# Performance work log

Measured on AMD Instinct MI355X. Metric: run time of the kernel, lower is better.

The kernel has to match this reference:

```python
import jax, jax.numpy as jnp
import numpy as np

B, N, D, E = 2, 50000, 64, 800000


def setup_inputs() -> dict:
    key = jax.random.key(0)
    k = jax.random.split(key, 6)
    return {
        "prev_embeddings": jax.random.normal(k[0], (B, N, D), dtype=jnp.float32),
        "edges_ij": jax.random.randint(k[1], (E, 2), 0, N, dtype=jnp.int64 if jax.config.jax_enable_x64 else jnp.int32),
        "node_features_embeddings": jax.random.normal(k[2], (B, N, D), dtype=jnp.float32),
        "edge_features_embeddings": jax.random.normal(k[3], (B, N, D), dtype=jnp.float32),
        "edge_status": jax.random.uniform(k[4], (E,), dtype=jnp.float32),
        "W": jax.random.normal(k[5], (D, D), dtype=jnp.float32) / np.sqrt(D).astype(np.float32),
    }


def reference(prev_embeddings, edges_ij, node_features_embeddings, edge_features_embeddings, edge_status, W):
    # prev_embeddings: (B, N, D); edges_ij: (E, 2); edge_status: (E,) in [0,1]; W: (D, D) theta2 weight (no bias)
    u = edges_ij[:, 0]
    v = edges_ij[:, 1]
    g = edge_status.astype(prev_embeddings.dtype).reshape(1, -1, 1)  # broadcast (1,E,1) over batch
    h_u = prev_embeddings[:, u, :] * g  # gather source endpoint, gate
    h_v = prev_embeddings[:, v, :] * g  # gather dest endpoint, gate
    # scatter-add gated messages in both directions: nbr[b, v] += h_u, nbr[b, u] += h_v
    nbr = jnp.zeros_like(prev_embeddings).at[:, v, :].add(h_u).at[:, u, :].add(h_v)
    x2 = jnp.einsum('bnd,ed->bne', nbr, W)  # Linear(D,D,bias=False): nbr @ W.T
    return jax.nn.leaky_relu(node_features_embeddings + x2 + edge_features_embeddings)
```

## Files before the change

kernel.cpp:

```cpp
#include <hip/hip_runtime.h>

constexpr int B = 2;
constexpr int N = 50000;
constexpr int D = 64;
constexpr int E = 800000;
constexpr int CAP = 96;
constexpr int XG = 8;
constexpr int NPG = N / XG;
constexpr int CSTRIDE_PAD = 16;

constexpr int ROWS_PER_WAVE = 25;
constexpr int BGROUPS = 1563;
constexpr int PGROUPS = 125;
constexpr int TOTAL_GROUPS = BGROUPS + PGROUPS;

__device__ __forceinline__ unsigned f2bf(float f) {
    unsigned u = __float_as_uint(f);
    return (u + 0x7FFFu + ((u >> 16) & 1u)) >> 16;
}
__device__ __forceinline__ float bfhi2f(unsigned bits) {
    return __uint_as_float(bits & 0xFFFF0000u);
}
__device__ __forceinline__ float bflo2f(unsigned bits) {
    return __uint_as_float(bits << 16);
}

__device__ __forceinline__ void acc8(float g, const uint4& r, float* a) {
    a[0] += g * bflo2f(r.x); a[1] += g * bfhi2f(r.x);
    a[2] += g * bflo2f(r.y); a[3] += g * bfhi2f(r.y);
    a[4] += g * bflo2f(r.z); a[5] += g * bfhi2f(r.z);
    a[6] += g * bflo2f(r.w); a[7] += g * bfhi2f(r.w);
}

__global__ __launch_bounds__(256) void build_pgemm_fused(
    const int2* __restrict__ edges, const float* __restrict__ status,
    int* __restrict__ counts, unsigned* __restrict__ slots,
    const float* __restrict__ prev, const float* __restrict__ W,
    unsigned* __restrict__ P32, int cstride)
{
    int grp = blockIdx.x >> 3;
    int sub8 = blockIdx.x & 7;
    int t = threadIdx.x;

    int cyc = grp / 13, pos = grp % 13;
    bool is_pgemm = (pos == 12) && (grp < PGROUPS * 13);

    if (!is_pgemm) {
        int b = (grp < PGROUPS * 13) ? (cyc * 12 + pos) : (1500 + (grp - PGROUPS * 13));
        int e0 = b * 512 + t;
        int e1 = e0 + 256;
        bool has1 = (e1 < E);

        int2 uv0 = edges[e0];
        float st0 = status[e0];
        int2 uv1 = has1 ? edges[e1] : uv0;
        float st1 = has1 ? status[e1] : 0.f;
        unsigned gb0 = f2bf(st0) << 16;
        unsigned gb1 = f2bf(st1) << 16;

        bool du0 = (uv0.x / NPG == sub8);
        bool dv0 = (uv0.y / NPG == sub8);
        bool du1 = has1 && (uv1.x / NPG == sub8);
        bool dv1 = has1 && (uv1.y / NPG == sub8);

        int pu0 = CAP, pv0 = CAP, pu1 = CAP, pv1 = CAP;
        if (du0) pu0 = atomicAdd(&counts[(size_t)uv0.x * cstride], 1);
        if (dv0) pv0 = atomicAdd(&counts[(size_t)uv0.y * cstride], 1);
        if (du1) pu1 = atomicAdd(&counts[(size_t)uv1.x * cstride], 1);
        if (dv1) pv1 = atomicAdd(&counts[(size_t)uv1.y * cstride], 1);
        if (du0 && pu0 < CAP) slots[(size_t)uv0.x * CAP + pu0] = gb0 | (unsigned)uv0.y;
        if (dv0 && pv0 < CAP) slots[(size_t)uv0.y * CAP + pv0] = gb0 | (unsigned)uv0.x;
        if (du1 && pu1 < CAP) slots[(size_t)uv1.x * CAP + pu1] = gb1 | (unsigned)uv1.y;
        if (dv1 && pv1 < CAP) slots[(size_t)uv1.y * CAP + pv1] = gb1 | (unsigned)uv1.x;
    } else {
        int pb = cyc * 8 + sub8;
        int wave = t >> 6, lane = t & 63;

        const float4* W4 = (const float4*)W;
        float4 w[16];
#pragma unroll
        for (int q = 0; q < 16; ++q) w[q] = W4[lane * 16 + q];

        int row0 = pb * (4 * ROWS_PER_WAVE) + wave * ROWS_PER_WAVE;
        for (int r = 0; r < ROWS_PER_WAVE; ++r) {
            int row = __builtin_amdgcn_readfirstlane(row0 + r);
            const float* pr = prev + (size_t)row * D;

            float acc = 0.f;
#pragma unroll
            for (int d = 0; d < D; ++d) {
                const float4& wq = w[d >> 2];
                float wd = (d & 3) == 0 ? wq.x : (d & 3) == 1 ? wq.y
                         : (d & 3) == 2 ? wq.z : wq.w;
                acc += pr[d] * wd;
            }

            float partner = __shfl_xor(acc, 1, 64);
            if ((lane & 1) == 0) {
                int bsel = row >= N;
                int n = row - bsel * N;
                P32[(size_t)n * 64 + bsel * 32 + (lane >> 1)]
                    = f2bf(acc) | (f2bf(partner) << 16);
            }
        }
    }
}

__global__ __launch_bounds__(256) void gather_final(
    const uint4* __restrict__ P4,
    const int* __restrict__ counts,
    const unsigned* __restrict__ slots,
    const float* __restrict__ node,
    const float* __restrict__ edgef,
    float* __restrict__ out, int cstride)
{
    __shared__ float xs[4][2][D];

    int t = threadIdx.x;
    int wave = t >> 6, lane = t & 63;
    int n = blockIdx.x * 4 + wave;
    int j = lane & 7;
    int sub = lane >> 3;

    size_t b0 = (size_t)n * D + lane;
    size_t b1 = (size_t)N * D + b0;
    float nd0 = __builtin_nontemporal_load(node + b0);
    float ef0 = __builtin_nontemporal_load(edgef + b0);
    float nd1 = __builtin_nontemporal_load(node + b1);
    float ef1 = __builtin_nontemporal_load(edgef + b1);

    int cnt = min(counts[(size_t)n * cstride], CAP);
    size_t sbase = (size_t)n * CAP;

    float a0[8], a1[8];
#pragma unroll
    for (int i = 0; i < 8; ++i) { a0[i] = 0.f; a1[i] = 0.f; }

    int last = cnt - 1;
    int nch = (cnt + 31) >> 5;
    for (int c = 0; c < nch; ++c) {
        int k0 = sub + c * 32;
        unsigned e0 = __builtin_nontemporal_load(slots + sbase + min(k0,      last));
        unsigned e1 = __builtin_nontemporal_load(slots + sbase + min(k0 + 8,  last));
        unsigned e2 = __builtin_nontemporal_load(slots + sbase + min(k0 + 16, last));
        unsigned e3 = __builtin_nontemporal_load(slots + sbase + min(k0 + 24, last));
        float g0 = (k0      < cnt) ? bfhi2f(e0) : 0.f;
        float g1 = (k0 + 8  < cnt) ? bfhi2f(e1) : 0.f;
        float g2 = (k0 + 16 < cnt) ? bfhi2f(e2) : 0.f;
        float g3 = (k0 + 24 < cnt) ? bfhi2f(e3) : 0.f;
        unsigned m0 = e0 & 0xFFFFu, m1 = e1 & 0xFFFFu;
        unsigned m2 = e2 & 0xFFFFu, m3 = e3 & 0xFFFFu;
        uint4 r00 = P4[(size_t)m0 * 16 + j];
        uint4 r10 = P4[(size_t)m0 * 16 + 8 + j];
        uint4 r01 = P4[(size_t)m1 * 16 + j];
        uint4 r11 = P4[(size_t)m1 * 16 + 8 + j];
        uint4 r02 = P4[(size_t)m2 * 16 + j];
        uint4 r12 = P4[(size_t)m2 * 16 + 8 + j];
        uint4 r03 = P4[(size_t)m3 * 16 + j];
        uint4 r13 = P4[(size_t)m3 * 16 + 8 + j];
        acc8(g0, r00, a0); acc8(g0, r10, a1);
        acc8(g1, r01, a0); acc8(g1, r11, a1);
        acc8(g2, r02, a0); acc8(g2, r12, a1);
        acc8(g3, r03, a0); acc8(g3, r13, a1);
    }

#pragma unroll
    for (int m = 8; m <= 32; m <<= 1) {
#pragma unroll
        for (int i = 0; i < 8; ++i) {
            a0[i] += __shfl_xor(a0[i], m, 64);
            a1[i] += __shfl_xor(a1[i], m, 64);
        }
    }

    if (sub == 0) {
        *(float4*)&xs[wave][0][j * 8]     = make_float4(a0[0], a0[1], a0[2], a0[3]);
        *(float4*)&xs[wave][0][j * 8 + 4] = make_float4(a0[4], a0[5], a0[6], a0[7]);
        *(float4*)&xs[wave][1][j * 8]     = make_float4(a1[0], a1[1], a1[2], a1[3]);
        *(float4*)&xs[wave][1][j * 8 + 4] = make_float4(a1[4], a1[5], a1[6], a1[7]);
    }
    float s0 = xs[wave][0][lane];
    float s1 = xs[wave][1][lane];

    float y0 = nd0 + s0 + ef0;
    float y1 = nd1 + s1 + ef1;
    float r0 = (y0 >= 0.f) ? y0 : 0.01f * y0;
    float r1 = (y1 >= 0.f) ? y1 : 0.01f * y1;
    __builtin_nontemporal_store(r0, out + b0);
    __builtin_nontemporal_store(r1, out + b1);
}

__device__ inline void atomic_add4(float* p, float4 val, float g) {
    atomicAdd(p + 0, val.x * g);
    atomicAdd(p + 1, val.y * g);
    atomicAdd(p + 2, val.z * g);
    atomicAdd(p + 3, val.w * g);
}

__global__ __launch_bounds__(256) void scatter_kernel(
    const float* __restrict__ prev,
    const int2* __restrict__ edges,
    const float* __restrict__ status,
    float* __restrict__ nbr)
{
    int idx = blockIdx.x * 256 + threadIdx.x;
    int e = idx >> 4;
    int q = idx & 15;
    if (e >= E) return;
    int2 uv = edges[e];
    float g = status[e];
    const float4* p0 = (const float4*)prev;
    const float4* p1 = (const float4*)(prev + (size_t)N * D);
    float4 pu0 = p0[(size_t)uv.x * 16 + q];
    float4 pv0 = p0[(size_t)uv.y * 16 + q];
    float4 pu1 = p1[(size_t)uv.x * 16 + q];
    float4 pv1 = p1[(size_t)uv.y * 16 + q];
    float* n0 = nbr;
    float* n1 = nbr + (size_t)N * D;
    int off_v = uv.y * D + q * 4;
    int off_u = uv.x * D + q * 4;
    atomic_add4(n0 + off_v, pu0, g);
    atomic_add4(n0 + off_u, pv0, g);
    atomic_add4(n1 + off_v, pu1, g);
    atomic_add4(n1 + off_u, pv1, g);
}

__global__ __launch_bounds__(256) void gemm_relu_kernel(
    float* __restrict__ out,
    const float* __restrict__ node,
    const float* __restrict__ edgef,
    const float* __restrict__ W)
{
    __shared__ float Wl[D][D + 1];
    __shared__ float xs[4][D];
    int t = threadIdx.x;
    for (int i = t; i < D * D; i += 256) Wl[i >> 6][i & 63] = W[i];
    int wave = t >> 6, lane = t & 63;
    int row = blockIdx.x * 4 + wave;
    size_t base = (size_t)row * D;
    float x = out[base + lane];
    xs[wave][lane] = x;
    __syncthreads();
    float acc = 0.f;
#pragma unroll
    for (int d = 0; d < D; ++d) acc += xs[wave][d] * Wl[lane][d];
    float y = node[base + lane] + acc + edgef[base + lane];
    out[base + lane] = (y >= 0.f) ? y : 0.01f * y;
}

extern "C" void kernel_launch(void* const* d_in, const int* in_sizes, int n_in,
                              void* d_out, int out_size, void* d_ws, size_t ws_size,
                              hipStream_t stream) {
    const float* prev   = (const float*)d_in[0];
    const int*   edges  = (const int*)d_in[1];
    const float* node   = (const float*)d_in[2];
    const float* edgef  = (const float*)d_in[3];
    const float* status = (const float*)d_in[4];
    const float* W      = (const float*)d_in[5];
    float* out = (float*)d_out;

    const int2* edges2 = (const int2*)edges;

    size_t slots_bytes  = (size_t)N * CAP * sizeof(unsigned);
    size_t p_bytes      = (size_t)N * 64 * sizeof(unsigned);
    size_t counts_pad   = (size_t)N * CSTRIDE_PAD * sizeof(int);
    size_t counts_min   = (size_t)N * sizeof(int);

    int cstride;
    size_t counts_bytes;
    if (ws_size >= slots_bytes + counts_pad + p_bytes) {
        cstride = CSTRIDE_PAD; counts_bytes = counts_pad;
    } else if (ws_size >= slots_bytes + counts_min + p_bytes) {
        cstride = 1; counts_bytes = counts_min;
    } else {
        hipMemsetAsync(out, 0, (size_t)B * N * D * sizeof(float), stream);
        scatter_kernel<<<(E * 16) / 256, 256, 0, stream>>>(prev, edges2, status, out);
        gemm_relu_kernel<<<(B * N) / 4, 256, 0, stream>>>(out, node, edgef, W);
        return;
    }

    unsigned* slots = (unsigned*)d_ws;
    int* counts = (int*)((char*)d_ws + slots_bytes);
    unsigned* P32 = (unsigned*)((char*)d_ws + slots_bytes + counts_bytes);

    hipMemsetAsync(counts, 0, counts_bytes, stream);
    build_pgemm_fused<<<TOTAL_GROUPS * 8, 256, 0, stream>>>(
        edges2, status, counts, slots, prev, W, P32, cstride);
    gather_final<<<N / 4, 256, 0, stream>>>(
        (const uint4*)P32, counts, slots, node, edgef, out, cstride);
}
```

Baseline: 260.5 us.

## Drop 8-way node-partitioned edge passes and rebalance fused build/pgemm block schedule

Previously each edge batch was read by 8 blocks, each handling only the endpoints that fall in its node range (presumably for atomic/L2 locality across XCDs). Now each edge batch is handled by a single block doing all atomics, which cuts the edge reads and block count roughly 8x. The pgemm share is retuned to 500 blocks of 50 rows per wave, interleaved one per three build blocks. The change trades locality-partitioned atomics and slot writes for fewer redundant edge loads and fewer blocks, at the risk of scattered cross-XCD atomic traffic.

Result: slower. 336.5 us (+29.2%).

```diff
diff --git a/kernel.cpp b/kernel.cpp
--- a/kernel.cpp
+++ b/kernel.cpp
@@ -5,14 +5,13 @@
 constexpr int D = 64;
 constexpr int E = 800000;
 constexpr int CAP = 96;
-constexpr int XG = 8;
-constexpr int NPG = N / XG;
 constexpr int CSTRIDE_PAD = 16;
 
-constexpr int ROWS_PER_WAVE = 25;
-constexpr int BGROUPS = 1563;
-constexpr int PGROUPS = 125;
-constexpr int TOTAL_GROUPS = BGROUPS + PGROUPS;
+constexpr int ROWS_PER_WAVE = 50;
+constexpr int BBLOCKS = 1563;
+constexpr int PBLOCKS2 = 500;
+constexpr int CYCLES = 521;
+constexpr int GRID = CYCLES * 4;
 
 __device__ __forceinline__ unsigned f2bf(float f) {
     unsigned u = __float_as_uint(f);
@@ -38,15 +37,12 @@
     const float* __restrict__ prev, const float* __restrict__ W,
     unsigned* __restrict__ P32, int cstride)
 {
-    int grp = blockIdx.x >> 3;
-    int sub8 = blockIdx.x & 7;
+    int cyc = blockIdx.x >> 2;
+    int pos = blockIdx.x & 3;
     int t = threadIdx.x;
 
-    int cyc = grp / 13, pos = grp % 13;
-    bool is_pgemm = (pos == 12) && (grp < PGROUPS * 13);
-
-    if (!is_pgemm) {
-        int b = (grp < PGROUPS * 13) ? (cyc * 12 + pos) : (1500 + (grp - PGROUPS * 13));
+    if (pos < 3) {
+        int b = cyc * 3 + pos;
         int e0 = b * 512 + t;
         int e1 = e0 + 256;
         bool has1 = (e1 < E);
@@ -58,22 +54,20 @@
         unsigned gb0 = f2bf(st0) << 16;
         unsigned gb1 = f2bf(st1) << 16;
 
-        bool du0 = (uv0.x / NPG == sub8);
-        bool dv0 = (uv0.y / NPG == sub8);
-        bool du1 = has1 && (uv1.x / NPG == sub8);
-        bool dv1 = has1 && (uv1.y / NPG == sub8);
-
-        int pu0 = CAP, pv0 = CAP, pu1 = CAP, pv1 = CAP;
-        if (du0) pu0 = atomicAdd(&counts[(size_t)uv0.x * cstride], 1);
-        if (dv0) pv0 = atomicAdd(&counts[(size_t)uv0.y * cstride], 1);
-        if (du1) pu1 = atomicAdd(&counts[(size_t)uv1.x * cstride], 1);
-        if (dv1) pv1 = atomicAdd(&counts[(size_t)uv1.y * cstride], 1);
-        if (du0 && pu0 < CAP) slots[(size_t)uv0.x * CAP + pu0] = gb0 | (unsigned)uv0.y;
-        if (dv0 && pv0 < CAP) slots[(size_t)uv0.y * CAP + pv0] = gb0 | (unsigned)uv0.x;
-        if (du1 && pu1 < CAP) slots[(size_t)uv1.x * CAP + pu1] = gb1 | (unsigned)uv1.y;
-        if (dv1 && pv1 < CAP) slots[(size_t)uv1.y * CAP + pv1] = gb1 | (unsigned)uv1.x;
+        int pu0 = atomicAdd(&counts[(size_t)uv0.x * cstride], 1);
+        int pv0 = atomicAdd(&counts[(size_t)uv0.y * cstride], 1);
+        int pu1 = CAP, pv1 = CAP;
+        if (has1) {
+            pu1 = atomicAdd(&counts[(size_t)uv1.x * cstride], 1);
+            pv1 = atomicAdd(&counts[(size_t)uv1.y * cstride], 1);
+        }
+        if (pu0 < CAP) slots[(size_t)uv0.x * CAP + pu0] = gb0 | (unsigned)uv0.y;
+        if (pv0 < CAP) slots[(size_t)uv0.y * CAP + pv0] = gb0 | (unsigned)uv0.x;
+        if (has1 && pu1 < CAP) slots[(size_t)uv1.x * CAP + pu1] = gb1 | (unsigned)uv1.y;
+        if (has1 && pv1 < CAP) slots[(size_t)uv1.y * CAP + pv1] = gb1 | (unsigned)uv1.x;
     } else {
-        int pb = cyc * 8 + sub8;
+        int pb = cyc;
+        if (pb >= PBLOCKS2) return;
         int wave = t >> 6, lane = t & 63;
 
         const float4* W4 = (const float4*)W;
@@ -284,7 +278,7 @@
     unsigned* P32 = (unsigned*)((char*)d_ws + slots_bytes + counts_bytes);
 
     hipMemsetAsync(counts, 0, counts_bytes, stream);
-    build_pgemm_fused<<<TOTAL_GROUPS * 8, 256, 0, stream>>>(
+    build_pgemm_fused<<<GRID, 256, 0, stream>>>(
         edges2, status, counts, slots, prev, W, P32, cstride);
     gather_final<<<N / 4, 256, 0, stream>>>(
         (const uint4*)P32, counts, slots, node, edgef, out, cstride);
```
